# Kernel tuning notes

Hardware: AMD Instinct MI355X
Metric: run time of the kernel (lower is better)

The kernel has to match this reference:

```python
import jax, jax.numpy as jnp
import numpy as np

BATCH, SEQ, FEAT, UNITS, OUT = 128, 2048, 64, 64, 6


def setup_inputs() -> dict:
    key = jax.random.key(0)
    ks = jax.random.split(key, 12)
    s = 0.05
    inp = {
        "x": jax.random.normal(ks[0], (BATCH, SEQ, FEAT), dtype=jnp.float32),
        # LSTMCell 0 (kernel, recurrent_kernel, bias); gate order i,f,g,o
        "W0": jax.random.normal(ks[1], (FEAT, 4 * UNITS), dtype=jnp.float32) * s,
        "U0": jax.random.normal(ks[2], (UNITS, 4 * UNITS), dtype=jnp.float32) * s,
        "b0": jax.random.normal(ks[3], (4 * UNITS,), dtype=jnp.float32) * s,
        # LSTMCell 1 (shared by layers 2 AND 3, as in the original code)
        "W1": jax.random.normal(ks[4], (UNITS, 4 * UNITS), dtype=jnp.float32) * s,
        "U1": jax.random.normal(ks[5], (UNITS, 4 * UNITS), dtype=jnp.float32) * s,
        "b1": jax.random.normal(ks[6], (4 * UNITS,), dtype=jnp.float32) * s,
        # Dense heads
        "Wf": jax.random.normal(ks[7], (UNITS, 64), dtype=jnp.float32) * s,
        "bf": jax.random.normal(ks[8], (64,), dtype=jnp.float32) * s,
        "Wo": jax.random.normal(ks[9], (64, OUT), dtype=jnp.float32) * s,
        "bo": jax.random.normal(ks[10], (OUT,), dtype=jnp.float32) * s,
    }
    return inp


def _lstm_cell(c, h, xin, W, U, b):
    # Keras LSTMCell math, gate order i, f, g(candidate), o
    z = xin @ W + h @ U + b  # [B, 4U]
    i, f, g, o = jnp.split(z, 4, axis=-1)
    c_new = jax.nn.sigmoid(f) * c + jax.nn.sigmoid(i) * jnp.tanh(g)
    h_new = jax.nn.sigmoid(o) * jnp.tanh(c_new)
    return c_new, h_new


def reference(x, W0, U0, b0, W1, U1, b1, Wf, bf, Wo, bo):
    B = x.shape[0]
    z = jnp.zeros((B, UNITS), dtype=x.dtype)
    init = (z, z, z, z, z, z)  # (c0,h0,c1,h1,c2,h2)

    def step(carry, xt):
        c0, h0, c1, h1, c2, h2 = carry
        c0, h0 = _lstm_cell(c0, h0, xt, W0, U0, b0)
        c1, h1 = _lstm_cell(c1, h1, h0, W1, U1, b1)
        # NOTE: original code reuses rnn_cell1's weights for the 3rd layer
        c2, h2 = _lstm_cell(c2, h2, h1, W1, U1, b1)
        return (c0, h0, c1, h1, c2, h2), None

    xt = jnp.swapaxes(x, 0, 1)  # [T, B, F]
    (c0, h0, c1, h1, c2, h2), _ = jax.lax.scan(step, init, xt)
    y = jax.nn.relu(h2 @ Wf + bf)
    return y @ Wo + bo
```

## Files before the change

kernel.cpp:

```cpp
#include <hip/hip_runtime.h>

#define BATCHN 128
#define SEQT   2048
#define FEAT   64
#define UNITS  64
#define NCOL   256
#define OUTD   6
#define CH     24
#define BUF    96
#define RING   8
#define PFD    6

typedef float v2f __attribute__((ext_vector_type(2)));

__device__ __forceinline__ float fast_exp2(float x) {
#if __has_builtin(__builtin_amdgcn_exp2f)
    return __builtin_amdgcn_exp2f(x);
#else
    return exp2f(x);
#endif
}
__device__ __forceinline__ float fast_rcp(float x) {
#if __has_builtin(__builtin_amdgcn_rcpf)
    return __builtin_amdgcn_rcpf(x);
#else
    return 1.0f / x;
#endif
}
__device__ __forceinline__ float sig_(float x) {
    return fast_rcp(1.0f + fast_exp2(-1.4426950408889634f * x));
}
__device__ __forceinline__ float tanh_(float x) {
    float xc = fminf(fmaxf(x, -15.0f), 15.0f);
    float e  = fast_exp2(2.8853900817779268f * xc);
    return (e - 1.0f) * fast_rcp(e + 1.0f);
}

__device__ __forceinline__ v2f pk_fma(v2f a, v2f b, v2f c) {
    return __builtin_elementwise_fma(a, b, c);
}

template<int CTRL>
__device__ __forceinline__ float dppf(float v) {
    return __builtin_bit_cast(float, __builtin_amdgcn_update_dpp(
        0, __builtin_bit_cast(int, v), CTRL, 0xF, 0xF, true));
}
__device__ __forceinline__ v2f red8v(v2f v) {
    v2f t;
    t.x = dppf<0xB1>(v.x);  t.y = dppf<0xB1>(v.y);  v = v + t;
    t.x = dppf<0x4E>(v.x);  t.y = dppf<0x4E>(v.y);  v = v + t;
    t.x = dppf<0x141>(v.x); t.y = dppf<0x141>(v.y); v = v + t;
    return v;
}

__device__ __forceinline__ void gload16(float* lds, const float* g) {
    __builtin_amdgcn_global_load_lds(
        (const __attribute__((address_space(1))) void*)g,
        (__attribute__((address_space(3))) void*)lds, 16, 0, 0);
}

__global__ __launch_bounds__(768, 3)
void lstm3_ring(const float* __restrict__ x,
                const float* __restrict__ W0, const float* __restrict__ U0,
                const float* __restrict__ b0,
                const float* __restrict__ W1, const float* __restrict__ U1,
                const float* __restrict__ b1,
                const float* __restrict__ Wf, const float* __restrict__ bfv,
                const float* __restrict__ Wo, const float* __restrict__ bov,
                float* __restrict__ out)
{
    const int b   = blockIdx.x;
    const int tid = threadIdx.x;
    const int grp = tid >> 8;
    const int lt  = tid & 255;
    const int cg  = lt >> 3;
    const int kg  = lt & 7;
    const int up  = kg & 1;
    const int myu = 2 * cg + up;

    __shared__ __align__(16) float ls[6 * BUF];
    __shared__ __align__(16) float lxr[RING][FEAT];
    __shared__ float lact[UNITS];
    float* const lsb = ls;

    const float* Wsel = (grp == 0) ? W0 : W1;
    const float* Usel = (grp == 0) ? U0 : U1;
    const float* bsel = (grp == 0) ? b0 : b1;
    const float* Msel = (kg < 4) ? Wsel : Usel;

    v2f wt[16][4];
    float biasv[4];
#pragma unroll
    for (int g = 0; g < 4; ++g) {
        const int colb = (g << 6) + 2 * cg;
#pragma unroll
        for (int k = 0; k < 16; ++k) {
            const int r = (kg & 3) * 16 + k;
            wt[k][g] = (v2f){Msel[r * NCOL + colb], Msel[r * NCOL + colb + 1]};
        }
        biasv[g] = bsel[(g << 6) + myu];
    }

    if (tid < 6 * BUF) lsb[tid] = 0.f;

    const float* xbase = x + (size_t)b * SEQT * FEAT;
    if (tid < 16) {
#pragma unroll
        for (int s = 0; s < PFD; ++s)
            gload16(&lxr[s][0], xbase + (size_t)s * FEAT + tid * 4);
    }
    __syncthreads();

    const float* inB0 = (grp == 0) ? lsb : (lsb + (2 * (grp - 1)) * BUF);
    const float* inB1 = inB0 + BUF;
    const float* rcB0 = lsb + (2 * grp) * BUF;
    const float* rcB1 = rcB0 + BUF;
    const int chOff = (kg & 3) * CH;
    const float* opP0 = ((kg < 4) ? inB0 : rcB0) + chOff;
    const float* opP1 = ((kg < 4) ? inB1 : rcB1) + chOff;
    const bool xlane = (grp == 0) && (kg < 4);

    float* hwp0 = lsb + (2 * grp) * BUF + CH * (myu >> 4) + (myu & 15);
    float* hwp1 = hwp0 + BUF;

    float c = 0.f;

#define MAC1(V, K)                                                            \
    { v2f s_; s_.x = (V); s_.y = (V);                                         \
      a0 = pk_fma(s_, wt[K][0], a0);                                          \
      a1 = pk_fma(s_, wt[K][1], a1);                                          \
      a2 = pk_fma(s_, wt[K][2], a2);                                          \
      a3 = pk_fma(s_, wt[K][3], a3); }

    for (int tk = 0; tk < SEQT + 2; ++tk) {
        if (tid < 16) {
            const int tn = tk + PFD;
            if (tn < SEQT)
                gload16(&lxr[tn & (RING - 1)][0],
                        xbase + (size_t)tn * FEAT + tid * 4);
        }

        const int t_ = tk - grp;
        if (t_ >= 0 && t_ < SEQT) {
            const float* op = (tk & 1) ? opP0 : opP1;
            if (xlane) op = &lxr[tk & (RING - 1)][kg * 16];

            float4 o0 = *(const float4*)(op);
            float4 o1 = *(const float4*)(op + 4);
            float4 o2 = *(const float4*)(op + 8);
            float4 o3 = *(const float4*)(op + 12);

            v2f a0 = (v2f){0.f, 0.f}, a1 = a0, a2 = a0, a3 = a0;
            MAC1(o0.x, 0)  MAC1(o0.y, 1)  MAC1(o0.z, 2)  MAC1(o0.w, 3)
            MAC1(o1.x, 4)  MAC1(o1.y, 5)  MAC1(o1.z, 6)  MAC1(o1.w, 7)
            MAC1(o2.x, 8)  MAC1(o2.y, 9)  MAC1(o2.z, 10) MAC1(o2.w, 11)
            MAC1(o3.x, 12) MAC1(o3.y, 13) MAC1(o3.z, 14) MAC1(o3.w, 15)

            v2f z0 = red8v(a0), z1 = red8v(a1), z2 = red8v(a2), z3 = red8v(a3);
            const float zi = (up ? z0.y : z0.x) + biasv[0];
            const float zf = (up ? z1.y : z1.x) + biasv[1];
            const float zg = (up ? z2.y : z2.x) + biasv[2];
            const float zo = (up ? z3.y : z3.x) + biasv[3];

            const float ig = sig_(zi), fg = sig_(zf);
            const float gg = tanh_(zg), og = sig_(zo);
            c = fg * c + ig * gg;
            const float hn = og * tanh_(c);
            if (kg < 2) *((tk & 1) ? hwp1 : hwp0) = hn;
        }

        if ((tid >> 6) == 0)
            asm volatile("s_waitcnt vmcnt(5)" ::: "memory");
        asm volatile("s_waitcnt lgkmcnt(0)\n\ts_barrier" ::: "memory");
    }
#undef MAC1

    const float* h2f = lsb + (2 * 2 + 1) * BUF;
    if (tid < UNITS) {
        float a = bfv[tid];
#pragma unroll
        for (int k = 0; k < UNITS; ++k)
            a += h2f[CH * (k >> 4) + (k & 15)] * Wf[k * 64 + tid];
        lact[tid] = fmaxf(a, 0.f);
    }
    __syncthreads();
    if (tid < OUTD) {
        float a = bov[tid];
#pragma unroll
        for (int k = 0; k < UNITS; ++k) a += lact[k] * Wo[k * OUTD + tid];
        out[b * OUTD + tid] = a;
    }
}

extern "C" void kernel_launch(void* const* d_in, const int* in_sizes, int n_in,
                              void* d_out, int out_size, void* d_ws, size_t ws_size,
                              hipStream_t stream) {
    const float* x   = (const float*)d_in[0];
    const float* W0  = (const float*)d_in[1];
    const float* U0  = (const float*)d_in[2];
    const float* b0  = (const float*)d_in[3];
    const float* W1  = (const float*)d_in[4];
    const float* U1  = (const float*)d_in[5];
    const float* b1  = (const float*)d_in[6];
    const float* Wf  = (const float*)d_in[7];
    const float* bfv = (const float*)d_in[8];
    const float* Wo  = (const float*)d_in[9];
    const float* bov = (const float*)d_in[10];
    float* out = (float*)d_out;

    lstm3_ring<<<BATCHN, 768, 0, stream>>>(x, W0, U0, b0, W1, U1, b1,
                                           Wf, bfv, Wo, bov, out);
}
```

Baseline: 2.138 ms.

## Replace per-step block barriers with LDS progress flags for dataflow layer pipelining

Drops the block-wide s_barrier that ran every time step. Each layer group now spins on per-group progress counters held in LDS, and the hidden states move into a 4-slot ring, so the three LSTM layers can run decoupled and skew ahead of one another. The goal is to stop the fastest group from waiting on the slowest at every step. In exchange it adds polling with s_sleep, atomic counters per wave, and relies on relaxed workgroup-scope atomics for memory ordering, which puts correctness at risk.

```diff
diff --git a/kernel.cpp b/kernel.cpp
--- a/kernel.cpp
+++ b/kernel.cpp
@@ -7,9 +7,9 @@
 #define NCOL   256
 #define OUTD   6
 #define CH     24
-#define BUF    96
-#define RING   8
-#define PFD    6
+#define SLOT   128
+#define XRING  8
+#define PFD    4
 
 typedef float v2f __attribute__((ext_vector_type(2)));
 
@@ -59,15 +59,19 @@
         (__attribute__((address_space(3))) void*)lds, 16, 0, 0);
 }
 
+__device__ __forceinline__ int ldflag(const int* p) {
+    return __hip_atomic_load(p, __ATOMIC_RELAXED, __HIP_MEMORY_SCOPE_WORKGROUP);
+}
+
 __global__ __launch_bounds__(768, 3)
-void lstm3_ring(const float* __restrict__ x,
-                const float* __restrict__ W0, const float* __restrict__ U0,
-                const float* __restrict__ b0,
-                const float* __restrict__ W1, const float* __restrict__ U1,
-                const float* __restrict__ b1,
-                const float* __restrict__ Wf, const float* __restrict__ bfv,
-                const float* __restrict__ Wo, const float* __restrict__ bov,
-                float* __restrict__ out)
+void lstm3_df(const float* __restrict__ x,
+              const float* __restrict__ W0, const float* __restrict__ U0,
+              const float* __restrict__ b0,
+              const float* __restrict__ W1, const float* __restrict__ U1,
+              const float* __restrict__ b1,
+              const float* __restrict__ Wf, const float* __restrict__ bfv,
+              const float* __restrict__ Wo, const float* __restrict__ bov,
+              float* __restrict__ out)
 {
     const int b   = blockIdx.x;
     const int tid = threadIdx.x;
@@ -77,11 +81,13 @@
     const int kg  = lt & 7;
     const int up  = kg & 1;
     const int myu = 2 * cg + up;
-
-    __shared__ __align__(16) float ls[6 * BUF];
-    __shared__ __align__(16) float lxr[RING][FEAT];
+    const int wv  = tid >> 6;
+
+    __shared__ __align__(16) float lh[3 * 4 * SLOT];
+    __shared__ __align__(16) float lxr[XRING * FEAT];
     __shared__ float lact[UNITS];
-    float* const lsb = ls;
+    __shared__ int prog[4];
+    __shared__ int cnt[3][2];
 
     const float* Wsel = (grp == 0) ? W0 : W1;
     const float* Usel = (grp == 0) ? U0 : U1;
@@ -101,81 +107,106 @@
         biasv[g] = bsel[(g << 6) + myu];
     }
 
-    if (tid < 6 * BUF) lsb[tid] = 0.f;
+    for (int i = tid; i < 3 * 4 * SLOT; i += 768) lh[i] = 0.f;
+    if (tid < 4) prog[tid] = -1;
+    if (tid < 6) (&cnt[0][0])[tid] = 0;
 
     const float* xbase = x + (size_t)b * SEQT * FEAT;
     if (tid < 16) {
 #pragma unroll
         for (int s = 0; s < PFD; ++s)
-            gload16(&lxr[s][0], xbase + (size_t)s * FEAT + tid * 4);
+            gload16(&lxr[s * FEAT], xbase + (size_t)s * FEAT + tid * 4);
     }
     __syncthreads();
 
-    const float* inB0 = (grp == 0) ? lsb : (lsb + (2 * (grp - 1)) * BUF);
-    const float* inB1 = inB0 + BUF;
-    const float* rcB0 = lsb + (2 * grp) * BUF;
-    const float* rcB1 = rcB0 + BUF;
-    const int chOff = (kg & 3) * CH;
-    const float* opP0 = ((kg < 4) ? inB0 : rcB0) + chOff;
-    const float* opP1 = ((kg < 4) ? inB1 : rcB1) + chOff;
-    const bool xlane = (grp == 0) && (kg < 4);
-
-    float* hwp0 = lsb + (2 * grp) * BUF + CH * (myu >> 4) + (myu & 15);
-    float* hwp1 = hwp0 + BUF;
+    const bool isFF = (kg < 4);
+    const bool xOp  = (grp == 0) && isFF;
+    const float* opB = isFF
+        ? ((grp == 0) ? (const float*)lxr
+                      : (&lh[(grp - 1) * 4 * SLOT] + (kg & 3) * CH))
+        : (&lh[grp * 4 * SLOT] + (kg & 3) * CH);
+    float* const hgrp = &lh[grp * 4 * SLOT];
+    const int hwoff = CH * (myu >> 4) + (myu & 15);
 
     float c = 0.f;
 
+#pragma unroll 1
+    for (int t = 0; t < SEQT; ++t) {
+        const int sW = t & 3, sR = (t + 3) & 3, sX = t & 7;
+
+        for (;;) {
+            bool ok = (ldflag(&prog[grp]) >= t - 1);
+            if (grp > 0) ok = ok && (ldflag(&prog[grp - 1]) >= t);
+            if (grp < 2) ok = ok && (ldflag(&prog[grp + 1]) >= t - 4);
+            if (grp == 0 && wv != 0) ok = ok && (ldflag(&prog[3]) >= t);
+            if (ok) break;
+            __builtin_amdgcn_s_sleep(1);
+        }
+        asm volatile("" ::: "memory");
+
+        if (wv == 0) {
+            if (t + PFD < SEQT) {
+                if (tid < 16)
+                    gload16(&lxr[((t + PFD) & 7) * FEAT],
+                            xbase + (size_t)(t + PFD) * FEAT + tid * 4);
+                asm volatile("s_waitcnt vmcnt(4)" ::: "memory");
+            } else if (t == SEQT - 4) { asm volatile("s_waitcnt vmcnt(3)" ::: "memory"); }
+            else if   (t == SEQT - 3) { asm volatile("s_waitcnt vmcnt(2)" ::: "memory"); }
+            else if   (t == SEQT - 2) { asm volatile("s_waitcnt vmcnt(1)" ::: "memory"); }
+            else                      { asm volatile("s_waitcnt vmcnt(0)" ::: "memory"); }
+            if (tid == 0)
+                __hip_atomic_store(&prog[3], t, __ATOMIC_RELAXED,
+                                   __HIP_MEMORY_SCOPE_WORKGROUP);
+        }
+
+        const float* op = xOp ? (lxr + sX * FEAT + kg * 16)
+                              : (opB + (isFF ? sW : sR) * SLOT);
+        float4 o0 = *(const float4*)(op);
+        float4 o1 = *(const float4*)(op + 4);
+        float4 o2 = *(const float4*)(op + 8);
+        float4 o3 = *(const float4*)(op + 12);
+
+        v2f a0 = (v2f){0.f, 0.f}, a1 = a0, a2 = a0, a3 = a0;
 #define MAC1(V, K)                                                            \
-    { v2f s_; s_.x = (V); s_.y = (V);                                         \
-      a0 = pk_fma(s_, wt[K][0], a0);                                          \
-      a1 = pk_fma(s_, wt[K][1], a1);                                          \
-      a2 = pk_fma(s_, wt[K][2], a2);                                          \
-      a3 = pk_fma(s_, wt[K][3], a3); }
-
-    for (int tk = 0; tk < SEQT + 2; ++tk) {
-        if (tid < 16) {
-            const int tn = tk + PFD;
-            if (tn < SEQT)
-                gload16(&lxr[tn & (RING - 1)][0],
-                        xbase + (size_t)tn * FEAT + tid * 4);
-        }
-
-        const int t_ = tk - grp;
-        if (t_ >= 0 && t_ < SEQT) {
-            const float* op = (tk & 1) ? opP0 : opP1;
-            if (xlane) op = &lxr[tk & (RING - 1)][kg * 16];
-
-            float4 o0 = *(const float4*)(op);
-            float4 o1 = *(const float4*)(op + 4);
-            float4 o2 = *(const float4*)(op + 8);
-            float4 o3 = *(const float4*)(op + 12);
-
-            v2f a0 = (v2f){0.f, 0.f}, a1 = a0, a2 = a0, a3 = a0;
-            MAC1(o0.x, 0)  MAC1(o0.y, 1)  MAC1(o0.z, 2)  MAC1(o0.w, 3)
-            MAC1(o1.x, 4)  MAC1(o1.y, 5)  MAC1(o1.z, 6)  MAC1(o1.w, 7)
-            MAC1(o2.x, 8)  MAC1(o2.y, 9)  MAC1(o2.z, 10) MAC1(o2.w, 11)
-            MAC1(o3.x, 12) MAC1(o3.y, 13) MAC1(o3.z, 14) MAC1(o3.w, 15)
-
-            v2f z0 = red8v(a0), z1 = red8v(a1), z2 = red8v(a2), z3 = red8v(a3);
-            const float zi = (up ? z0.y : z0.x) + biasv[0];
-            const float zf = (up ? z1.y : z1.x) + biasv[1];
-            const float zg = (up ? z2.y : z2.x) + biasv[2];
-            const float zo = (up ? z3.y : z3.x) + biasv[3];
-
-            const float ig = sig_(zi), fg = sig_(zf);
-            const float gg = tanh_(zg), og = sig_(zo);
-            c = fg * c + ig * gg;
-            const float hn = og * tanh_(c);
-            if (kg < 2) *((tk & 1) ? hwp1 : hwp0) = hn;
-        }
-
-        if ((tid >> 6) == 0)
-            asm volatile("s_waitcnt vmcnt(5)" ::: "memory");
-        asm volatile("s_waitcnt lgkmcnt(0)\n\ts_barrier" ::: "memory");
-    }
+        { v2f s_; s_.x = (V); s_.y = (V);                                     \
+          a0 = pk_fma(s_, wt[K][0], a0);                                      \
+          a1 = pk_fma(s_, wt[K][1], a1);                                      \
+          a2 = pk_fma(s_, wt[K][2], a2);                                      \
+          a3 = pk_fma(s_, wt[K][3], a3); }
+        MAC1(o0.x, 0)  MAC1(o0.y, 1)  MAC1(o0.z, 2)  MAC1(o0.w, 3)
+        MAC1(o1.x, 4)  MAC1(o1.y, 5)  MAC1(o1.z, 6)  MAC1(o1.w, 7)
+        MAC1(o2.x, 8)  MAC1(o2.y, 9)  MAC1(o2.z, 10) MAC1(o2.w, 11)
+        MAC1(o3.x, 12) MAC1(o3.y, 13) MAC1(o3.z, 14) MAC1(o3.w, 15)
 #undef MAC1
 
-    const float* h2f = lsb + (2 * 2 + 1) * BUF;
+        v2f z0 = red8v(a0), z1 = red8v(a1), z2 = red8v(a2), z3 = red8v(a3);
+        const float zi = (up ? z0.y : z0.x) + biasv[0];
+        const float zf = (up ? z1.y : z1.x) + biasv[1];
+        const float zg = (up ? z2.y : z2.x) + biasv[2];
+        const float zo = (up ? z3.y : z3.x) + biasv[3];
+
+        const float ig = sig_(zi), fg = sig_(zf);
+        const float gg = tanh_(zg), og = sig_(zo);
+        c = fg * c + ig * gg;
+        const float hn = og * tanh_(c);
+        if (kg < 2) hgrp[sW * SLOT + hwoff] = hn;
+
+        asm volatile("" ::: "memory");
+        if ((lt & 63) == 0) {
+            int old = __hip_atomic_fetch_add(&cnt[grp][t & 1], 1,
+                        __ATOMIC_RELAXED, __HIP_MEMORY_SCOPE_WORKGROUP);
+            if (old == 3) {
+                __hip_atomic_store(&cnt[grp][t & 1], 0, __ATOMIC_RELAXED,
+                                   __HIP_MEMORY_SCOPE_WORKGROUP);
+                __hip_atomic_store(&prog[grp], t, __ATOMIC_RELAXED,
+                                   __HIP_MEMORY_SCOPE_WORKGROUP);
+            }
+        }
+    }
+
+    __syncthreads();
+
+    const float* h2f = &lh[(2 * 4 + 3) * SLOT];
     if (tid < UNITS) {
         float a = bfv[tid];
 #pragma unroll
@@ -208,6 +239,6 @@
     const float* bov = (const float*)d_in[10];
     float* out = (float*)d_out;
 
-    lstm3_ring<<<BATCHN, 768, 0, stream>>>(x, W0, U0, b0, W1, U1, b1,
-                                           Wf, bfv, Wo, bov, out);
-}
+    lstm3_df<<<BATCHN, 768, 0, stream>>>(x, W0, U0, b0, W1, U1, b1,
+                                         Wf, bfv, Wo, bov, out);
+}
```

Result: slower. 2.529 ms (+18.3%).

## Switch recurrent matvec to fp16 packed dot products with half-precision state buffers

Applied to the files above, without the earlier changes.

Weights are stored as packed fp16 pairs in registers, and the per-step matvec uses v_dot2 (fdot2) with fp32 accumulation in place of packed fp32 FMAs. The hidden-state exchange buffers in LDS now hold fp16 pairs, with neighbouring units combined via DPP before one packed store. The tanh is simplified to a sigmoid-style form, and the prefetch wait counts are tuned per wave near the sequence end. The aim is to halve the FMA instruction count and the LDS traffic on the serial critical path, at the cost of fp16 rounding error in the weights and the recurrent state over 2048 steps.

```diff
diff --git a/kernel.cpp b/kernel.cpp
--- a/kernel.cpp
+++ b/kernel.cpp
@@ -6,12 +6,13 @@
 #define UNITS  64
 #define NCOL   256
 #define OUTD   6
-#define CH     24
-#define BUF    96
 #define RING   8
 #define PFD    6
+#define CHB    48
+#define HBUF   192
 
 typedef float v2f __attribute__((ext_vector_type(2)));
+typedef __fp16 hv2 __attribute__((ext_vector_type(2)));
 
 __device__ __forceinline__ float fast_exp2(float x) {
 #if __has_builtin(__builtin_amdgcn_exp2f)
@@ -31,13 +32,20 @@
     return fast_rcp(1.0f + fast_exp2(-1.4426950408889634f * x));
 }
 __device__ __forceinline__ float tanh_(float x) {
-    float xc = fminf(fmaxf(x, -15.0f), 15.0f);
-    float e  = fast_exp2(2.8853900817779268f * xc);
-    return (e - 1.0f) * fast_rcp(e + 1.0f);
-}
-
-__device__ __forceinline__ v2f pk_fma(v2f a, v2f b, v2f c) {
-    return __builtin_elementwise_fma(a, b, c);
+    float e = fast_exp2(-2.8853900817779268f * x);
+    return fmaf(2.0f, fast_rcp(1.0f + e), -1.0f);
+}
+
+__device__ __forceinline__ float fdot2_(hv2 a, hv2 b, float c) {
+#if __has_builtin(__builtin_amdgcn_fdot2)
+    return __builtin_amdgcn_fdot2(a, b, c, false);
+#else
+    return fmaf((float)a.x, (float)b.x, fmaf((float)a.y, (float)b.y, c));
+#endif
+}
+
+__device__ __forceinline__ hv2 cvtpk_(float a, float b) {
+    return __builtin_amdgcn_cvt_pkrtz(a, b);
 }
 
 template<int CTRL>
@@ -60,14 +68,14 @@
 }
 
 __global__ __launch_bounds__(768, 3)
-void lstm3_ring(const float* __restrict__ x,
-                const float* __restrict__ W0, const float* __restrict__ U0,
-                const float* __restrict__ b0,
-                const float* __restrict__ W1, const float* __restrict__ U1,
-                const float* __restrict__ b1,
-                const float* __restrict__ Wf, const float* __restrict__ bfv,
-                const float* __restrict__ Wo, const float* __restrict__ bov,
-                float* __restrict__ out)
+void lstm3_h16(const float* __restrict__ x,
+               const float* __restrict__ W0, const float* __restrict__ U0,
+               const float* __restrict__ b0,
+               const float* __restrict__ W1, const float* __restrict__ U1,
+               const float* __restrict__ b1,
+               const float* __restrict__ Wf, const float* __restrict__ bfv,
+               const float* __restrict__ Wo, const float* __restrict__ bov,
+               float* __restrict__ out)
 {
     const int b   = blockIdx.x;
     const int tid = threadIdx.x;
@@ -77,86 +85,125 @@
     const int kg  = lt & 7;
     const int up  = kg & 1;
     const int myu = 2 * cg + up;
-
-    __shared__ __align__(16) float ls[6 * BUF];
-    __shared__ __align__(16) float lxr[RING][FEAT];
+    const int wv  = tid >> 6;
+
+    __shared__ __align__(16) unsigned char lhb[6 * HBUF];
+    __shared__ __align__(16) float lxr[RING * FEAT];
     __shared__ float lact[UNITS];
-    float* const lsb = ls;
 
     const float* Wsel = (grp == 0) ? W0 : W1;
     const float* Usel = (grp == 0) ? U0 : U1;
     const float* bsel = (grp == 0) ? b0 : b1;
     const float* Msel = (kg < 4) ? Wsel : Usel;
 
-    v2f wt[16][4];
+    hv2 wt[4][2][8];
     float biasv[4];
 #pragma unroll
     for (int g = 0; g < 4; ++g) {
         const int colb = (g << 6) + 2 * cg;
 #pragma unroll
-        for (int k = 0; k < 16; ++k) {
-            const int r = (kg & 3) * 16 + k;
-            wt[k][g] = (v2f){Msel[r * NCOL + colb], Msel[r * NCOL + colb + 1]};
+        for (int j = 0; j < 8; ++j) {
+            const int r = (kg & 3) * 16 + 2 * j;
+            hv2 w0p, w1p;
+            w0p.x = (__fp16)Msel[r * NCOL + colb];
+            w0p.y = (__fp16)Msel[(r + 1) * NCOL + colb];
+            w1p.x = (__fp16)Msel[r * NCOL + colb + 1];
+            w1p.y = (__fp16)Msel[(r + 1) * NCOL + colb + 1];
+            wt[g][0][j] = w0p;
+            wt[g][1][j] = w1p;
         }
         biasv[g] = bsel[(g << 6) + myu];
     }
 
-    if (tid < 6 * BUF) lsb[tid] = 0.f;
+    if (tid < 6 * HBUF / 4) ((unsigned int*)lhb)[tid] = 0u;
 
     const float* xbase = x + (size_t)b * SEQT * FEAT;
     if (tid < 16) {
 #pragma unroll
         for (int s = 0; s < PFD; ++s)
-            gload16(&lxr[s][0], xbase + (size_t)s * FEAT + tid * 4);
+            gload16(&lxr[s * FEAT], xbase + (size_t)s * FEAT + tid * 4);
     }
     __syncthreads();
 
-    const float* inB0 = (grp == 0) ? lsb : (lsb + (2 * (grp - 1)) * BUF);
-    const float* inB1 = inB0 + BUF;
-    const float* rcB0 = lsb + (2 * grp) * BUF;
-    const float* rcB1 = rcB0 + BUF;
-    const int chOff = (kg & 3) * CH;
-    const float* opP0 = ((kg < 4) ? inB0 : rcB0) + chOff;
-    const float* opP1 = ((kg < 4) ? inB1 : rcB1) + chOff;
-    const bool xlane = (grp == 0) && (kg < 4);
-
-    float* hwp0 = lsb + (2 * grp) * BUF + CH * (myu >> 4) + (myu & 15);
-    float* hwp1 = hwp0 + BUF;
+    const bool isFF = (kg < 4);
+    const bool xOp  = (grp == 0) && isFF;
+    const int ffb   = (grp == 0) ? 0 : (grp - 1);
+    const unsigned char* opP0 =
+        lhb + ((isFF ? ffb : grp) * 2 + 0) * HBUF + (kg & 3) * CHB;
+    const unsigned char* opP1 = opP0 + HBUF;
+
+    unsigned char* hwP0 = lhb + (grp * 2 + 0) * HBUF + (cg >> 3) * CHB + (cg & 7) * 4;
+    unsigned char* hwP1 = hwP0 + HBUF;
 
     float c = 0.f;
 
-#define MAC1(V, K)                                                            \
-    { v2f s_; s_.x = (V); s_.y = (V);                                         \
-      a0 = pk_fma(s_, wt[K][0], a0);                                          \
-      a1 = pk_fma(s_, wt[K][1], a1);                                          \
-      a2 = pk_fma(s_, wt[K][2], a2);                                          \
-      a3 = pk_fma(s_, wt[K][3], a3); }
-
     for (int tk = 0; tk < SEQT + 2; ++tk) {
-        if (tid < 16) {
-            const int tn = tk + PFD;
-            if (tn < SEQT)
-                gload16(&lxr[tn & (RING - 1)][0],
-                        xbase + (size_t)tn * FEAT + tid * 4);
+        const int p = tk & 1;
+
+        if (wv == 0) {
+            if (tk + PFD < SEQT) {
+                if (tid < 16)
+                    gload16(&lxr[((tk + PFD) & (RING - 1)) * FEAT],
+                            xbase + (size_t)(tk + PFD) * FEAT + tid * 4);
+                asm volatile("s_waitcnt vmcnt(5)" ::: "memory");
+            }
+            else if (tk == SEQT - 6) { asm volatile("s_waitcnt vmcnt(4)" ::: "memory"); }
+            else if (tk == SEQT - 5) { asm volatile("s_waitcnt vmcnt(3)" ::: "memory"); }
+            else if (tk == SEQT - 4) { asm volatile("s_waitcnt vmcnt(2)" ::: "memory"); }
+            else if (tk == SEQT - 3) { asm volatile("s_waitcnt vmcnt(1)" ::: "memory"); }
+            else                     { asm volatile("s_waitcnt vmcnt(0)" ::: "memory"); }
         }
 
         const int t_ = tk - grp;
         if (t_ >= 0 && t_ < SEQT) {
-            const float* op = (tk & 1) ? opP0 : opP1;
-            if (xlane) op = &lxr[tk & (RING - 1)][kg * 16];
-
-            float4 o0 = *(const float4*)(op);
-            float4 o1 = *(const float4*)(op + 4);
-            float4 o2 = *(const float4*)(op + 8);
-            float4 o3 = *(const float4*)(op + 12);
-
-            v2f a0 = (v2f){0.f, 0.f}, a1 = a0, a2 = a0, a3 = a0;
-            MAC1(o0.x, 0)  MAC1(o0.y, 1)  MAC1(o0.z, 2)  MAC1(o0.w, 3)
-            MAC1(o1.x, 4)  MAC1(o1.y, 5)  MAC1(o1.z, 6)  MAC1(o1.w, 7)
-            MAC1(o2.x, 8)  MAC1(o2.y, 9)  MAC1(o2.z, 10) MAC1(o2.w, 11)
-            MAC1(o3.x, 12) MAC1(o3.y, 13) MAC1(o3.z, 14) MAC1(o3.w, 15)
-
-            v2f z0 = red8v(a0), z1 = red8v(a1), z2 = red8v(a2), z3 = red8v(a3);
+            hv2 op[8];
+            if (xOp) {
+                const float* xp = lxr + (tk & (RING - 1)) * FEAT + (kg & 3) * 16;
+                float4 q0 = *(const float4*)(xp);
+                float4 q1 = *(const float4*)(xp + 4);
+                float4 q2 = *(const float4*)(xp + 8);
+                float4 q3 = *(const float4*)(xp + 12);
+                op[0] = cvtpk_(q0.x, q0.y);
+                op[1] = cvtpk_(q0.z, q0.w);
+                op[2] = cvtpk_(q1.x, q1.y);
+                op[3] = cvtpk_(q1.z, q1.w);
+                op[4] = cvtpk_(q2.x, q2.y);
+                op[5] = cvtpk_(q2.z, q2.w);
+                op[6] = cvtpk_(q3.x, q3.y);
+                op[7] = cvtpk_(q3.z, q3.w);
+            } else {
+                const unsigned char* ob = p ? opP0 : opP1;
+                uint4 r0 = *(const uint4*)(ob);
+                uint4 r1 = *(const uint4*)(ob + 16);
+                op[0] = __builtin_bit_cast(hv2, r0.x);
+                op[1] = __builtin_bit_cast(hv2, r0.y);
+                op[2] = __builtin_bit_cast(hv2, r0.z);
+                op[3] = __builtin_bit_cast(hv2, r0.w);
+                op[4] = __builtin_bit_cast(hv2, r1.x);
+                op[5] = __builtin_bit_cast(hv2, r1.y);
+                op[6] = __builtin_bit_cast(hv2, r1.z);
+                op[7] = __builtin_bit_cast(hv2, r1.w);
+            }
+
+            float acc[4][2];
+#pragma unroll
+            for (int g = 0; g < 4; ++g) { acc[g][0] = 0.f; acc[g][1] = 0.f; }
+#pragma unroll
+            for (int j = 0; j < 8; ++j) {
+#pragma unroll
+                for (int g = 0; g < 4; ++g) {
+                    acc[g][0] = fdot2_(op[j], wt[g][0][j], acc[g][0]);
+                    acc[g][1] = fdot2_(op[j], wt[g][1][j], acc[g][1]);
+                }
+            }
+
+            v2f z0, z1, z2, z3;
+            z0.x = acc[0][0]; z0.y = acc[0][1];
+            z1.x = acc[1][0]; z1.y = acc[1][1];
+            z2.x = acc[2][0]; z2.y = acc[2][1];
+            z3.x = acc[3][0]; z3.y = acc[3][1];
+            z0 = red8v(z0); z1 = red8v(z1); z2 = red8v(z2); z3 = red8v(z3);
+
             const float zi = (up ? z0.y : z0.x) + biasv[0];
             const float zf = (up ? z1.y : z1.x) + biasv[1];
             const float zg = (up ? z2.y : z2.x) + biasv[2];
@@ -166,21 +213,24 @@
             const float gg = tanh_(zg), og = sig_(zo);
             c = fg * c + ig * gg;
             const float hn = og * tanh_(c);
-            if (kg < 2) *((tk & 1) ? hwp1 : hwp0) = hn;
+
+            const float hother = dppf<0xF5>(hn);
+            if (kg == 0) {
+                hv2 hp = cvtpk_(hn, hother);
+                *(unsigned int*)(p ? hwP1 : hwP0) =
+                    __builtin_bit_cast(unsigned int, hp);
+            }
         }
 
-        if ((tid >> 6) == 0)
-            asm volatile("s_waitcnt vmcnt(5)" ::: "memory");
         asm volatile("s_waitcnt lgkmcnt(0)\n\ts_barrier" ::: "memory");
     }
-#undef MAC1
-
-    const float* h2f = lsb + (2 * 2 + 1) * BUF;
+
+    const __fp16* h2f = (const __fp16*)(lhb + 5 * HBUF);
     if (tid < UNITS) {
         float a = bfv[tid];
 #pragma unroll
         for (int k = 0; k < UNITS; ++k)
-            a += h2f[CH * (k >> 4) + (k & 15)] * Wf[k * 64 + tid];
+            a += (float)h2f[(k >> 4) * 24 + (k & 15)] * Wf[k * 64 + tid];
         lact[tid] = fmaxf(a, 0.f);
     }
     __syncthreads();
@@ -208,6 +258,6 @@
     const float* bov = (const float*)d_in[10];
     float* out = (float*)d_out;
 
-    lstm3_ring<<<BATCHN, 768, 0, stream>>>(x, W0, U0, b0, W1, U1, b1,
-                                           Wf, bfv, Wo, bov, out);
-}
+    lstm3_h16<<<BATCHN, 768, 0, stream>>>(x, W0, U0, b0, W1, U1, b1,
+                                          Wf, bfv, Wo, bov, out);
+}
```

After: 1.996 ms. -6.6%, faster.
